# Kernel optimization log

Hardware: AMD Instinct MI355X
Metric: run time of the kernel (lower is better)

## Reference

```python
import jax, jax.numpy as jnp
import numpy as np

INNER_DIM = 64
NUM_LABELS = 16
BIG_NEG = 1e12


def setup_inputs() -> dict:
    key = jax.random.key(0)
    k1, k2 = jax.random.split(key)
    B, S, H = 8, 512, 768
    sequence_output = jax.random.normal(k1, (B, S, H), dtype=jnp.float32)
    attention_mask = jnp.ones((B, S), dtype=jnp.int32)
    W = jax.random.normal(k2, (NUM_LABELS * INNER_DIM * 2, H), dtype=jnp.float32) * 0.02
    b = jnp.zeros((NUM_LABELS * INNER_DIM * 2,), dtype=jnp.float32)
    return {"sequence_output": sequence_output, "attention_mask": attention_mask,
            "W": W, "b": b}


def _rope_sincos(seq_len, dim, dtype):
    # interleaved sinusoidal embedding: [sin0,cos0,sin1,cos1,...]
    pos = jnp.arange(seq_len, dtype=dtype)[:, None]              # [S,1]
    idx = jnp.arange(dim // 2, dtype=dtype)
    theta = jnp.power(jnp.asarray(1000.0, dtype), -2.0 * idx / dim)
    ang = pos * theta                                            # [S, dim/2]
    # cos_pos/sin_pos after repeat_interleave(2): [c0,c0,c1,c1,...]
    cos_pos = jnp.repeat(jnp.cos(ang), 2, axis=-1)               # [S, dim]
    sin_pos = jnp.repeat(jnp.sin(ang), 2, axis=-1)               # [S, dim]
    return sin_pos, cos_pos


def _rotate_half_interleaved(x):
    # stack([-x[...,1::2], x[...,::2]], -1).reshape(x.shape)
    x2 = jnp.stack([-x[..., 1::2], x[..., ::2]], axis=-1)
    return x2.reshape(x.shape)


def reference(sequence_output, attention_mask, W, b):
    B, S, H = sequence_output.shape
    L, D = NUM_LABELS, INNER_DIM
    # dense projection then split into per-label q/k: [B,S,L,2D]
    out = (sequence_output @ W.T + b).reshape(B, S, L, 2 * D)
    qw, kw = out[..., :D], out[..., D:]                          # [B,S,L,D]

    sin_pos, cos_pos = _rope_sincos(S, D, sequence_output.dtype)
    cos_pos = cos_pos[None, :, None, :]                          # [1,S,1,D]
    sin_pos = sin_pos[None, :, None, :]
    qw = qw * cos_pos + _rotate_half_interleaved(qw) * sin_pos
    kw = kw * cos_pos + _rotate_half_interleaved(kw) * sin_pos

    logits = jnp.einsum('bmhd,bnhd->bhmn', qw, kw)               # [B,L,S,S]

    pad = attention_mask.astype(logits.dtype)[:, None, None, :]  # [B,1,1,S]
    logits = logits * pad - (1.0 - pad) * BIG_NEG

    tril = jnp.tril(jnp.ones((S, S), dtype=logits.dtype), -1)    # strictly lower
    logits = logits - tril * BIG_NEG
    return logits / (D ** 0.5)
```

## Files before the change

kernel.cpp:

```cpp
#include <hip/hip_runtime.h>
#include <hip/hip_bf16.h>

typedef __bf16 bf16;
typedef __attribute__((ext_vector_type(8))) __bf16 bf16x8;
typedef __attribute__((ext_vector_type(4))) float f32x4;

#define BIG_NEG 1000000000000.0f
#define NEG_LOG_STEP 0.21586735253866545f

#define GLOAD_LDS16(g, l)                                                     \
    __builtin_amdgcn_global_load_lds(                                         \
        (const __attribute__((address_space(1))) void*)(g),                   \
        (__attribute__((address_space(3))) void*)(l), 16, 0, 0)

static __device__ inline uint2 pack4_bf16(float4 v) {
    union { bf16 h[4]; uint2 u; } t;
    t.h[0] = (bf16)v.x; t.h[1] = (bf16)v.y; t.h[2] = (bf16)v.z; t.h[3] = (bf16)v.w;
    return t.u;
}

__global__ __launch_bounds__(256) void convert_kernel(
    const float* __restrict__ X, const float* __restrict__ W,
    bf16* __restrict__ Xb, bf16* __restrict__ Wb)
{
    const int NX8 = (8 * 512 * 768) / 8;
    int idx = blockIdx.x * 256 + threadIdx.x;
    const float* src; bf16* dst; int i;
    if (idx < NX8) { src = X; dst = Xb; i = idx; }
    else           { src = W; dst = Wb; i = idx - NX8; }
    float4 a = reinterpret_cast<const float4*>(src)[i * 2];
    float4 b = reinterpret_cast<const float4*>(src)[i * 2 + 1];
    uint2 lo = pack4_bf16(a), hi = pack4_bf16(b);
    uint4 o; o.x = lo.x; o.y = lo.y; o.z = hi.x; o.w = hi.y;
    reinterpret_cast<uint4*>(dst)[i] = o;
}

__global__ __launch_bounds__(256) void proj_rope_kernel(
    const bf16* __restrict__ A, const bf16* __restrict__ B,
    const float* __restrict__ bias,
    bf16* __restrict__ q_ws, bf16* __restrict__ k_ws)
{
    const int K = 768;
    __shared__ __align__(16) bf16 As[128][32];
    __shared__ __align__(16) bf16 Bs[128][32];

    const int tid  = threadIdx.x;
    const int lane = tid & 63;
    const int wave = tid >> 6;
    const int wr   = wave >> 1;
    const int wc   = wave & 1;
    const int brow = blockIdx.x * 128;
    const int bcol = blockIdx.y * 128;
    const int lane15 = lane & 15;
    const int kq = (lane >> 4) * 8;
    const int srow = lane >> 2;
    const int scol = (lane & 3) * 8;

    f32x4 acc[4][4] = {};

    for (int k0 = 0; k0 < K; k0 += 32) {
        #pragma unroll
        for (int p = 0; p < 2; ++p) {
            int r0 = p * 64 + wave * 16;
            GLOAD_LDS16(A + (size_t)(brow + r0 + srow) * K + k0 + scol, &As[r0][0]);
            GLOAD_LDS16(B + (size_t)(bcol + r0 + srow) * K + k0 + scol, &Bs[r0][0]);
        }
        __syncthreads();

        bf16x8 af[4], bfv[4];
        #pragma unroll
        for (int mf = 0; mf < 4; ++mf)
            af[mf] = *reinterpret_cast<bf16x8*>(&As[wr * 64 + mf * 16 + lane15][kq]);
        #pragma unroll
        for (int nf = 0; nf < 4; ++nf)
            bfv[nf] = *reinterpret_cast<bf16x8*>(&Bs[wc * 64 + nf * 16 + lane15][kq]);
        #pragma unroll
        for (int mf = 0; mf < 4; ++mf)
            #pragma unroll
            for (int nf = 0; nf < 4; ++nf)
                acc[mf][nf] = __builtin_amdgcn_mfma_f32_16x16x32_bf16(
                    af[mf], bfv[nf], acc[mf][nf], 0, 0, 0);
        __syncthreads();
    }

    const int rowbase = brow + wr * 64 + (lane >> 4) * 4;
    const int colbase = bcol + wc * 64;
    #pragma unroll
    for (int nf = 0; nf < 4; ++nf) {
        int n = colbase + nf * 16 + lane15;
        int d = n & 127;
        int l = n >> 7;
        int p = (d & 63) >> 1;
        float theta = __expf(-(float)p * NEG_LOG_STEP);
        float bn = bias[n];
        bool odd = (d & 1) != 0;
        bf16* dst = (d < 64) ? q_ws : k_ws;
        int dd = d & 63;
        #pragma unroll
        for (int mf = 0; mf < 4; ++mf) {
            f32x4 v4 = acc[mf][nf];
            #pragma unroll
            for (int r = 0; r < 4; ++r) {
                int m = rowbase + mf * 16 + r;
                float v  = v4[r] + bn;
                float pv = __shfl_xor(v, 1);
                int s = m & 511;
                int b = m >> 9;
                float ang = (float)s * theta;
                float sn, cs;
                __sincosf(ang, &sn, &cs);
                float o = odd ? (v * cs + pv * sn) : (v * cs - pv * sn);
                dst[(((size_t)(b * 16 + l) * 512) + s) * 64 + dd] = (bf16)o;
            }
        }
    }
}

__global__ __launch_bounds__(256) void attn_kernel(
    const bf16* __restrict__ q_ws, const bf16* __restrict__ k_ws,
    const int* __restrict__ mask, float* __restrict__ out)
{
    __shared__ __align__(16) bf16 Qs[128][72];
    __shared__ __align__(16) bf16 Ks[128][72];

    const int tid  = threadIdx.x;
    const int lane = tid & 63;
    const int wave = tid >> 6;
    const int wr   = wave >> 1;
    const int wc   = wave & 1;
    const int bl   = blockIdx.z;
    const int brow = blockIdx.x * 128;
    const int bcol = blockIdx.y * 128;
    const int lane15 = lane & 15;

    const bf16* qbase = q_ws + (size_t)bl * 512 * 64;
    const bf16* kbase = k_ws + (size_t)bl * 512 * 64;

    #pragma unroll
    for (int pass = 0; pass < 4; ++pass) {
        int e   = (pass * 256 + tid) * 8;
        int row = e >> 6;
        int col = e & 63;
        *reinterpret_cast<uint4*>(&Qs[row][col]) =
            *reinterpret_cast<const uint4*>(&qbase[(size_t)(brow + row) * 64 + col]);
        *reinterpret_cast<uint4*>(&Ks[row][col]) =
            *reinterpret_cast<const uint4*>(&kbase[(size_t)(bcol + row) * 64 + col]);
    }
    __syncthreads();

    f32x4 acc[4][4] = {};
    #pragma unroll
    for (int ks = 0; ks < 2; ++ks) {
        int kq = ks * 32 + (lane >> 4) * 8;
        bf16x8 af[4], bfv[4];
        #pragma unroll
        for (int mf = 0; mf < 4; ++mf)
            af[mf] = *reinterpret_cast<bf16x8*>(&Qs[wr * 64 + mf * 16 + lane15][kq]);
        #pragma unroll
        for (int nf = 0; nf < 4; ++nf)
            bfv[nf] = *reinterpret_cast<bf16x8*>(&Ks[wc * 64 + nf * 16 + lane15][kq]);
        #pragma unroll
        for (int mf = 0; mf < 4; ++mf)
            #pragma unroll
            for (int nf = 0; nf < 4; ++nf)
                acc[mf][nf] = __builtin_amdgcn_mfma_f32_16x16x32_bf16(
                    af[mf], bfv[nf], acc[mf][nf], 0, 0, 0);
    }

    const int b = bl >> 4;
    const int* mrow = mask + b * 512;
    const int rowbase = brow + wr * 64 + (lane >> 4) * 4;
    const int colbase = bcol + wc * 64;
    #pragma unroll
    for (int nf = 0; nf < 4; ++nf) {
        int n = colbase + nf * 16 + lane15;
        float pf = (float)mrow[n];
        float mterm = (1.0f - pf) * BIG_NEG;
        #pragma unroll
        for (int mf = 0; mf < 4; ++mf) {
            f32x4 v4 = acc[mf][nf];
            #pragma unroll
            for (int r = 0; r < 4; ++r) {
                int m = rowbase + mf * 16 + r;
                float v = v4[r] * pf - mterm - ((m > n) ? BIG_NEG : 0.0f);
                out[((size_t)bl * 512 + m) * 512 + n] = v * 0.125f;
            }
        }
    }
}

extern "C" void kernel_launch(void* const* d_in, const int* in_sizes, int n_in,
                              void* d_out, int out_size, void* d_ws, size_t ws_size,
                              hipStream_t stream) {
    const float* X    = (const float*)d_in[0];
    const int*   mask = (const int*)d_in[1];
    const float* W    = (const float*)d_in[2];
    const float* bias = (const float*)d_in[3];

    float* out = (float*)d_out;

    bf16* q_ws = (bf16*)d_ws;
    bf16* k_ws = q_ws + (size_t)8 * 16 * 512 * 64;

    bf16* Xb = (bf16*)d_out;
    bf16* Wb = Xb + (size_t)8 * 512 * 768;

    const int NX8 = (8 * 512 * 768) / 8;
    const int NW8 = (2048 * 768) / 8;
    convert_kernel<<<(NX8 + NW8) / 256, 256, 0, stream>>>(X, W, Xb, Wb);
    proj_rope_kernel<<<dim3(32, 16), 256, 0, stream>>>(Xb, Wb, bias, q_ws, k_ws);
    attn_kernel<<<dim3(4, 4, 128), 256, 0, stream>>>(q_ws, k_ws, mask, out);
}
```

Measured before the change: 67.20 us.

## Transpose MFMA output layout for vectorized stores and skip masked attention tiles

Swaps the MFMA operand order in both GEMM kernels so each lane holds four consecutive columns, which allows vectorized 8-byte bf16 stores in the RoPE epilogue and 16-byte float4 stores of the logits. Fully masked lower-triangle tiles in the attention kernel skip the QK matmul and write only the constant mask value. The attention kernel now loads Q and K fragments straight from global memory instead of staging them in LDS, and the convert kernel and output stores use nontemporal hints. Together these aim to cut store transactions, LDS traffic and wasted MFMA work. The trade-off is less coalesced global fragment loads in the attention kernel.

```diff
diff --git a/kernel.cpp b/kernel.cpp
--- a/kernel.cpp
+++ b/kernel.cpp
@@ -4,17 +4,21 @@
 typedef __bf16 bf16;
 typedef __attribute__((ext_vector_type(8))) __bf16 bf16x8;
 typedef __attribute__((ext_vector_type(4))) float f32x4;
+typedef __attribute__((ext_vector_type(4))) int i32x4;
+typedef __attribute__((ext_vector_type(2))) unsigned int u32x2;
+typedef __attribute__((ext_vector_type(4))) unsigned int u32x4;
 
 #define BIG_NEG 1000000000000.0f
 #define NEG_LOG_STEP 0.21586735253866545f
+#define EXP_NEG_STEP 0.8058421877614818f
 
 #define GLOAD_LDS16(g, l)                                                     \
     __builtin_amdgcn_global_load_lds(                                         \
         (const __attribute__((address_space(1))) void*)(g),                   \
         (__attribute__((address_space(3))) void*)(l), 16, 0, 0)
 
-static __device__ inline uint2 pack4_bf16(float4 v) {
-    union { bf16 h[4]; uint2 u; } t;
+static __device__ inline u32x2 pack4_bf16(f32x4 v) {
+    union { bf16 h[4]; u32x2 u; } t;
     t.h[0] = (bf16)v.x; t.h[1] = (bf16)v.y; t.h[2] = (bf16)v.z; t.h[3] = (bf16)v.w;
     return t.u;
 }
@@ -28,11 +32,11 @@
     const float* src; bf16* dst; int i;
     if (idx < NX8) { src = X; dst = Xb; i = idx; }
     else           { src = W; dst = Wb; i = idx - NX8; }
-    float4 a = reinterpret_cast<const float4*>(src)[i * 2];
-    float4 b = reinterpret_cast<const float4*>(src)[i * 2 + 1];
-    uint2 lo = pack4_bf16(a), hi = pack4_bf16(b);
-    uint4 o; o.x = lo.x; o.y = lo.y; o.z = hi.x; o.w = hi.y;
-    reinterpret_cast<uint4*>(dst)[i] = o;
+    f32x4 a = __builtin_nontemporal_load(reinterpret_cast<const f32x4*>(src) + i * 2);
+    f32x4 b = __builtin_nontemporal_load(reinterpret_cast<const f32x4*>(src) + i * 2 + 1);
+    u32x2 lo = pack4_bf16(a), hi = pack4_bf16(b);
+    u32x4 o; o.x = lo.x; o.y = lo.y; o.z = hi.x; o.w = hi.y;
+    reinterpret_cast<u32x4*>(dst)[i] = o;
 }
 
 __global__ __launch_bounds__(256) void proj_rope_kernel(
@@ -75,43 +79,46 @@
         for (int nf = 0; nf < 4; ++nf)
             bfv[nf] = *reinterpret_cast<bf16x8*>(&Bs[wc * 64 + nf * 16 + lane15][kq]);
         #pragma unroll
-        for (int mf = 0; mf < 4; ++mf)
+        for (int nf = 0; nf < 4; ++nf)
             #pragma unroll
-            for (int nf = 0; nf < 4; ++nf)
-                acc[mf][nf] = __builtin_amdgcn_mfma_f32_16x16x32_bf16(
-                    af[mf], bfv[nf], acc[mf][nf], 0, 0, 0);
+            for (int mf = 0; mf < 4; ++mf)
+                acc[nf][mf] = __builtin_amdgcn_mfma_f32_16x16x32_bf16(
+                    bfv[nf], af[mf], acc[nf][mf], 0, 0, 0);
         __syncthreads();
     }
 
-    const int rowbase = brow + wr * 64 + (lane >> 4) * 4;
-    const int colbase = bcol + wc * 64;
+    const int mb = brow + wr * 64 + lane15;
+    const int nb = bcol + wc * 64 + (lane >> 4) * 4;
     #pragma unroll
     for (int nf = 0; nf < 4; ++nf) {
-        int n = colbase + nf * 16 + lane15;
-        int d = n & 127;
-        int l = n >> 7;
-        int p = (d & 63) >> 1;
-        float theta = __expf(-(float)p * NEG_LOG_STEP);
-        float bn = bias[n];
-        bool odd = (d & 1) != 0;
-        bf16* dst = (d < 64) ? q_ws : k_ws;
-        int dd = d & 63;
+        int n0 = nb + nf * 16;
+        int d0 = n0 & 127;
+        int l  = n0 >> 7;
+        int dd = d0 & 63;
+        int p0 = dd >> 1;
+        float th0 = __expf(-(float)p0 * NEG_LOG_STEP);
+        float th1 = th0 * EXP_NEG_STEP;
+        f32x4 bn = *reinterpret_cast<const f32x4*>(&bias[n0]);
+        bf16* dst = (d0 < 64) ? q_ws : k_ws;
         #pragma unroll
         for (int mf = 0; mf < 4; ++mf) {
-            f32x4 v4 = acc[mf][nf];
-            #pragma unroll
-            for (int r = 0; r < 4; ++r) {
-                int m = rowbase + mf * 16 + r;
-                float v  = v4[r] + bn;
-                float pv = __shfl_xor(v, 1);
-                int s = m & 511;
-                int b = m >> 9;
-                float ang = (float)s * theta;
-                float sn, cs;
-                __sincosf(ang, &sn, &cs);
-                float o = odd ? (v * cs + pv * sn) : (v * cs - pv * sn);
-                dst[(((size_t)(b * 16 + l) * 512) + s) * 64 + dd] = (bf16)o;
-            }
+            int m = mb + mf * 16;
+            int s = m & 511;
+            int b = m >> 9;
+            float fs = (float)s;
+            f32x4 a = acc[nf][mf];
+            float v0 = a.x + bn.x, v1 = a.y + bn.y;
+            float v2 = a.z + bn.z, v3 = a.w + bn.w;
+            float sn0, cs0, sn1, cs1;
+            __sincosf(fs * th0, &sn0, &cs0);
+            __sincosf(fs * th1, &sn1, &cs1);
+            union { bf16 h[4]; u32x2 u; } t;
+            t.h[0] = (bf16)(v0 * cs0 - v1 * sn0);
+            t.h[1] = (bf16)(v1 * cs0 + v0 * sn0);
+            t.h[2] = (bf16)(v2 * cs1 - v3 * sn1);
+            t.h[3] = (bf16)(v3 * cs1 + v2 * sn1);
+            *reinterpret_cast<u32x2*>(
+                &dst[(((size_t)(b * 16 + l) * 512) + s) * 64 + dd]) = t.u;
         }
     }
 }
@@ -120,9 +127,6 @@
     const bf16* __restrict__ q_ws, const bf16* __restrict__ k_ws,
     const int* __restrict__ mask, float* __restrict__ out)
 {
-    __shared__ __align__(16) bf16 Qs[128][72];
-    __shared__ __align__(16) bf16 Ks[128][72];
-
     const int tid  = threadIdx.x;
     const int lane = tid & 63;
     const int wave = tid >> 6;
@@ -131,60 +135,76 @@
     const int bl   = blockIdx.z;
     const int brow = blockIdx.x * 128;
     const int bcol = blockIdx.y * 128;
-    const int lane15 = lane & 15;
+    const int b    = bl >> 4;
+    const int* mrow = mask + b * 512;
+    float* obase = out + (size_t)bl * 512 * 512;
+
+    if (brow >= bcol + 128) {
+        int cg = tid & 31;
+        int n0 = bcol + cg * 4;
+        i32x4 mi = *reinterpret_cast<const i32x4*>(&mrow[n0]);
+        f32x4 o;
+        o.x = (-(1.0f - (float)mi.x) * BIG_NEG - BIG_NEG) * 0.125f;
+        o.y = (-(1.0f - (float)mi.y) * BIG_NEG - BIG_NEG) * 0.125f;
+        o.z = (-(1.0f - (float)mi.z) * BIG_NEG - BIG_NEG) * 0.125f;
+        o.w = (-(1.0f - (float)mi.w) * BIG_NEG - BIG_NEG) * 0.125f;
+        int r0 = tid >> 5;
+        #pragma unroll
+        for (int i = 0; i < 16; ++i) {
+            int row = brow + i * 8 + r0;
+            __builtin_nontemporal_store(
+                o, reinterpret_cast<f32x4*>(&obase[(size_t)row * 512 + n0]));
+        }
+        return;
+    }
 
     const bf16* qbase = q_ws + (size_t)bl * 512 * 64;
     const bf16* kbase = k_ws + (size_t)bl * 512 * 64;
-
-    #pragma unroll
-    for (int pass = 0; pass < 4; ++pass) {
-        int e   = (pass * 256 + tid) * 8;
-        int row = e >> 6;
-        int col = e & 63;
-        *reinterpret_cast<uint4*>(&Qs[row][col]) =
-            *reinterpret_cast<const uint4*>(&qbase[(size_t)(brow + row) * 64 + col]);
-        *reinterpret_cast<uint4*>(&Ks[row][col]) =
-            *reinterpret_cast<const uint4*>(&kbase[(size_t)(bcol + row) * 64 + col]);
-    }
-    __syncthreads();
+    const int lane15 = lane & 15;
+    const int kq = (lane >> 4) * 8;
 
     f32x4 acc[4][4] = {};
     #pragma unroll
     for (int ks = 0; ks < 2; ++ks) {
-        int kq = ks * 32 + (lane >> 4) * 8;
-        bf16x8 af[4], bfv[4];
+        bf16x8 qf[4], kf[4];
         #pragma unroll
         for (int mf = 0; mf < 4; ++mf)
-            af[mf] = *reinterpret_cast<bf16x8*>(&Qs[wr * 64 + mf * 16 + lane15][kq]);
-        #pragma unroll
-        for (int nf = 0; nf < 4; ++nf)
-            bfv[nf] = *reinterpret_cast<bf16x8*>(&Ks[wc * 64 + nf * 16 + lane15][kq]);
-        #pragma unroll
-        for (int mf = 0; mf < 4; ++mf)
+            qf[mf] = *reinterpret_cast<const bf16x8*>(
+                &qbase[(size_t)(brow + wr * 64 + mf * 16 + lane15) * 64 + ks * 32 + kq]);
+        #pragma unroll
+        for (int nf = 0; nf < 4; ++nf)
+            kf[nf] = *reinterpret_cast<const bf16x8*>(
+                &kbase[(size_t)(bcol + wc * 64 + nf * 16 + lane15) * 64 + ks * 32 + kq]);
+        #pragma unroll
+        for (int nf = 0; nf < 4; ++nf)
             #pragma unroll
-            for (int nf = 0; nf < 4; ++nf)
-                acc[mf][nf] = __builtin_amdgcn_mfma_f32_16x16x32_bf16(
-                    af[mf], bfv[nf], acc[mf][nf], 0, 0, 0);
-    }
-
-    const int b = bl >> 4;
-    const int* mrow = mask + b * 512;
-    const int rowbase = brow + wr * 64 + (lane >> 4) * 4;
-    const int colbase = bcol + wc * 64;
+            for (int mf = 0; mf < 4; ++mf)
+                acc[nf][mf] = __builtin_amdgcn_mfma_f32_16x16x32_bf16(
+                    kf[nf], qf[mf], acc[nf][mf], 0, 0, 0);
+    }
+
+    const int nb = bcol + wc * 64 + (lane >> 4) * 4;
+    const int mbase = brow + wr * 64 + lane15;
     #pragma unroll
     for (int nf = 0; nf < 4; ++nf) {
-        int n = colbase + nf * 16 + lane15;
-        float pf = (float)mrow[n];
-        float mterm = (1.0f - pf) * BIG_NEG;
+        int n0 = nb + nf * 16;
+        i32x4 mi = *reinterpret_cast<const i32x4*>(&mrow[n0]);
+        f32x4 pf; pf.x = (float)mi.x; pf.y = (float)mi.y;
+        pf.z = (float)mi.z; pf.w = (float)mi.w;
+        f32x4 mt;
+        mt.x = (1.0f - pf.x) * BIG_NEG; mt.y = (1.0f - pf.y) * BIG_NEG;
+        mt.z = (1.0f - pf.z) * BIG_NEG; mt.w = (1.0f - pf.w) * BIG_NEG;
         #pragma unroll
         for (int mf = 0; mf < 4; ++mf) {
-            f32x4 v4 = acc[mf][nf];
-            #pragma unroll
-            for (int r = 0; r < 4; ++r) {
-                int m = rowbase + mf * 16 + r;
-                float v = v4[r] * pf - mterm - ((m > n) ? BIG_NEG : 0.0f);
-                out[((size_t)bl * 512 + m) * 512 + n] = v * 0.125f;
-            }
+            int m = mbase + mf * 16;
+            f32x4 a = acc[nf][mf];
+            f32x4 o;
+            o.x = (a.x * pf.x - mt.x - ((m > n0 + 0) ? BIG_NEG : 0.0f)) * 0.125f;
+            o.y = (a.y * pf.y - mt.y - ((m > n0 + 1) ? BIG_NEG : 0.0f)) * 0.125f;
+            o.z = (a.z * pf.z - mt.z - ((m > n0 + 2) ? BIG_NEG : 0.0f)) * 0.125f;
+            o.w = (a.w * pf.w - mt.w - ((m > n0 + 3) ? BIG_NEG : 0.0f)) * 0.125f;
+            __builtin_nontemporal_store(
+                o, reinterpret_cast<f32x4*>(&obase[(size_t)m * 512 + n0]));
         }
     }
 }
```

Result: slower. 71.17 us (+5.9%).
